# Kernel optimization log

Measured on AMD Instinct MI355X. Metric: run time of the kernel, lower is better.

## Reference

```python
import jax, jax.numpy as jnp
import numpy as np

B, D, CL, QL = 32, 128, 1024, 512


def setup_inputs() -> dict:
    key = jax.random.key(0)
    kC, kQ, kW = jax.random.split(key, 3)
    C = jax.random.normal(kC, (B, D, CL), dtype=jnp.float32)
    Q = jax.random.normal(kQ, (B, D, QL), dtype=jnp.float32)
    # xavier_normal_ on (B*CL, 1, 3D): std = sqrt(2 / (fan_in + fan_out)) = sqrt(2/(1+3D))
    std = (2.0 / (1.0 + 3.0 * D)) ** 0.5
    W = jax.random.normal(kW, (B * CL, 1, 3 * D), dtype=jnp.float32) * std
    return {"C": C, "Q": Q, "W": W}


def reference(C, Q, W):
    # C: (B, D, CL), Q: (B, D, QL), W: (B*CL, 1, 3D)
    b, d, cl = C.shape
    Ct = jnp.transpose(C, (0, 2, 1))   # (B, CL, D)
    Qt = jnp.transpose(Q, (0, 2, 1))   # (B, QL, D)
    Wr = W.reshape(b, cl, 3 * d)
    wq, wc, wqc = Wr[..., :d], Wr[..., d:2 * d], Wr[..., 2 * d:]
    # Trilinear similarity: S[b,c,q] = wq[b,c].Q[b,q] + wc[b,c].C[b,c] + wqc[b,c].(C[b,c]*Q[b,q])
    S = (jnp.einsum('bcd,bqd->bcq', wq, Qt)
         + jnp.sum(wc * Ct, axis=-1, keepdims=True)
         + jnp.einsum('bcd,bqd->bcq', wqc * Ct, Qt))   # (B, CL, QL)
    S1 = jax.nn.softmax(S, axis=2)  # over queries
    S2 = jax.nn.softmax(S, axis=1)  # over context
    A = jnp.einsum('bcq,bqd->bcd', S1, Qt)             # (B, CL, D)
    # B = (S1 @ S2^T) @ C, reassociated as S1 @ (S2^T @ C) to avoid (CL,CL) intermediate
    S2tC = jnp.einsum('bkq,bkd->bqd', S2, Ct)          # (B, QL, D)
    Bm = jnp.einsum('bcq,bqd->bcd', S1, S2tC)          # (B, CL, D)
    out = jnp.concatenate([Ct, A, Ct * A, Ct * Bm], axis=2)  # (B, CL, 4D)
    # dropout is identity in eval mode
    return jnp.transpose(out, (0, 2, 1))               # (B, 4D, CL)
```

## Files before the change

### kernel.cpp

```cpp
#include <hip/hip_runtime.h>
#include <hip/hip_bf16.h>
#include <cstddef>

#define B_  32
#define D_  128
#define CL_ 1024
#define QL_ 512

using short8  = __attribute__((ext_vector_type(8))) short;
using short4v = __attribute__((ext_vector_type(4))) short;
using float4v = __attribute__((ext_vector_type(4))) float;

__device__ __forceinline__ unsigned short f2bf(float f) {
    unsigned int u = __float_as_uint(f);
    u += 0x7FFFu + ((u >> 16) & 1u);
    return (unsigned short)(u >> 16);
}
__device__ __forceinline__ float bf2f(unsigned short h) {
    return __uint_as_float(((unsigned int)h) << 16);
}

__global__ __launch_bounds__(256) void k_u_bias(const float* __restrict__ C,
                                                const float* __restrict__ W,
                                                unsigned short* __restrict__ U,
                                                float* __restrict__ bias,
                                                unsigned short* __restrict__ Cbf) {
    int b  = blockIdx.y;
    int c0 = blockIdx.x * 32;
    int tid = threadIdx.x;

    __shared__ float tile[128][33];
    __shared__ float bred[32][9];

    for (int pass = 0; pass < 16; ++pass) {
        int d = pass * 8 + (tid >> 5);
        int c = tid & 31;
        float v = C[((size_t)(b * D_ + d)) * CL_ + c0 + c];
        tile[d][c] = v;
        Cbf[((size_t)(b * D_ + d)) * CL_ + c0 + c] = f2bf(v);
    }
    __syncthreads();

    int tc    = tid >> 3;
    int lane8 = tid & 7;
    int c     = c0 + tc;
    size_t wbase = ((size_t)(b * CL_ + c)) * (3 * D_);
    size_t ubase = ((size_t)(b * CL_ + c)) * D_;

    float bpart = 0.f;
    #pragma unroll
    for (int i = 0; i < 4; ++i) {
        int d = i * 32 + lane8 * 4;
        float4 wq4  = *(const float4*)(W + wbase + d);
        float4 wc4  = *(const float4*)(W + wbase + D_ + d);
        float4 wqc4 = *(const float4*)(W + wbase + 2 * D_ + d);
        float ct0 = tile[d + 0][tc], ct1 = tile[d + 1][tc];
        float ct2 = tile[d + 2][tc], ct3 = tile[d + 3][tc];
        short4v u;
        u[0] = (short)f2bf(wq4.x + wqc4.x * ct0);
        u[1] = (short)f2bf(wq4.y + wqc4.y * ct1);
        u[2] = (short)f2bf(wq4.z + wqc4.z * ct2);
        u[3] = (short)f2bf(wq4.w + wqc4.w * ct3);
        *(short4v*)(U + ubase + d) = u;
        bpart += wc4.x * ct0 + wc4.y * ct1 + wc4.z * ct2 + wc4.w * ct3;
    }
    bred[tc][lane8] = bpart;
    __syncthreads();
    if (lane8 == 0) {
        float s = 0.f;
        for (int i = 0; i < 8; ++i) s += bred[tc][i];
        bias[b * CL_ + c] = s;
    }
}

__global__ __launch_bounds__(256) void k_qt(const float* __restrict__ Q,
                                            unsigned short* __restrict__ Qt,
                                            unsigned short* __restrict__ Qbf) {
    int b  = blockIdx.z;
    int d0 = blockIdx.y * 64;
    int q0 = blockIdx.x * 64;
    int tid = threadIdx.x;
    __shared__ float t[64][65];
    for (int p = 0; p < 16; ++p) {
        int d = p * 4 + (tid >> 6);
        int q = tid & 63;
        float v = Q[((size_t)(b * D_ + d0 + d)) * QL_ + q0 + q];
        t[d][q] = v;
        Qbf[((size_t)(b * D_ + d0 + d)) * QL_ + q0 + q] = f2bf(v);
    }
    __syncthreads();
    for (int p = 0; p < 16; ++p) {
        int q  = p * 4 + (tid >> 6);
        int dd = tid & 63;
        Qt[((size_t)(b * QL_ + q0 + q)) * D_ + d0 + dd] = f2bf(t[dd][q]);
    }
}

__global__ __launch_bounds__(256) void k_gs2(const unsigned short* __restrict__ Ubf,
                                             const unsigned short* __restrict__ Qtbf,
                                             const float* __restrict__ bias,
                                             unsigned short* __restrict__ Sbf,
                                             float* __restrict__ rmax,
                                             float* __restrict__ rinv,
                                             float* __restrict__ pcmax,
                                             float* __restrict__ pcsum) {
    int mt = blockIdx.x;
    int b  = blockIdx.y;
    int m0 = mt * 64;
    int tid  = threadIdx.x;
    int lane = tid & 63, wave = tid >> 6;
    int wm = wave >> 1, wn = wave & 1;
    int quad = lane >> 4, l15 = lane & 15;

    __shared__ __align__(16) short As[64][136];
    __shared__ __align__(16) short Bs[64][136];
    __shared__ float sbias[64];
    __shared__ float rmw[2][64], rsw[2][64];
    __shared__ float cmw[2][64], csw[2][64];

    const unsigned short* Ab = Ubf  + ((size_t)(b * CL_ + m0)) * D_;
    const unsigned short* Bb = Qtbf + ((size_t)(b * QL_)) * D_;

    #pragma unroll
    for (int i = 0; i < 4; ++i) {
        int flat = tid + i * 256;
        int row = flat >> 4, col = (flat & 15) * 8;
        *(short8*)&As[row][col] = *(const short8*)(Ab + (size_t)row * D_ + col);
    }
    if (tid < 64) sbias[tid] = bias[b * CL_ + m0 + tid];

    float rm_run[2][4], rs_run[2][4];
    #pragma unroll
    for (int fi = 0; fi < 2; ++fi)
        #pragma unroll
        for (int rr = 0; rr < 4; ++rr) { rm_run[fi][rr] = -1e30f; rs_run[fi][rr] = 0.f; }

    for (int chunk = 0; chunk < 8; ++chunk) {
        __syncthreads();
        #pragma unroll
        for (int i = 0; i < 4; ++i) {
            int flat = tid + i * 256;
            int row = flat >> 4, col = (flat & 15) * 8;
            *(short8*)&Bs[row][col] = *(const short8*)(Bb + (size_t)(chunk * 64 + row) * D_ + col);
        }
        __syncthreads();

        float4v acc[2][2] = {};
        #pragma unroll
        for (int ks = 0; ks < 128; ks += 32) {
            short8 af0 = *(const short8*)&As[wm * 32 + l15][ks + quad * 8];
            short8 af1 = *(const short8*)&As[wm * 32 + 16 + l15][ks + quad * 8];
            short8 bf0 = *(const short8*)&Bs[wn * 32 + l15][ks + quad * 8];
            short8 bf1 = *(const short8*)&Bs[wn * 32 + 16 + l15][ks + quad * 8];
            acc[0][0] = __builtin_amdgcn_mfma_f32_16x16x32_bf16(af0, bf0, acc[0][0], 0, 0, 0);
            acc[0][1] = __builtin_amdgcn_mfma_f32_16x16x32_bf16(af0, bf1, acc[0][1], 0, 0, 0);
            acc[1][0] = __builtin_amdgcn_mfma_f32_16x16x32_bf16(af1, bf0, acc[1][0], 0, 0, 0);
            acc[1][1] = __builtin_amdgcn_mfma_f32_16x16x32_bf16(af1, bf1, acc[1][1], 0, 0, 0);
        }

        float v[2][2][4];
        #pragma unroll
        for (int fi = 0; fi < 2; ++fi)
            #pragma unroll
            for (int fj = 0; fj < 2; ++fj)
                #pragma unroll
                for (int rr = 0; rr < 4; ++rr) {
                    int mloc = wm * 32 + fi * 16 + quad * 4 + rr;
                    float x = acc[fi][fj][rr] + sbias[mloc];
                    v[fi][fj][rr] = x;
                    int nloc = wn * 32 + fj * 16 + l15;
                    Sbf[((size_t)(b * CL_ + m0 + mloc)) * QL_ + chunk * 64 + nloc] = f2bf(x);
                }

        #pragma unroll
        for (int fi = 0; fi < 2; ++fi)
            #pragma unroll
            for (int rr = 0; rr < 4; ++rr) {
                float v0 = v[fi][0][rr], v1 = v[fi][1][rr];
                float nm = fmaxf(rm_run[fi][rr], fmaxf(v0, v1));
                rs_run[fi][rr] = rs_run[fi][rr] * __expf(rm_run[fi][rr] - nm)
                               + __expf(v0 - nm) + __expf(v1 - nm);
                rm_run[fi][rr] = nm;
            }

        #pragma unroll
        for (int fj = 0; fj < 2; ++fj) {
            float cm = v[0][fj][0];
            #pragma unroll
            for (int fi = 0; fi < 2; ++fi)
                #pragma unroll
                for (int rr = 0; rr < 4; ++rr) cm = fmaxf(cm, v[fi][fj][rr]);
            float cs = 0.f;
            #pragma unroll
            for (int fi = 0; fi < 2; ++fi)
                #pragma unroll
                for (int rr = 0; rr < 4; ++rr) cs += __expf(v[fi][fj][rr] - cm);
            #pragma unroll
            for (int off = 16; off <= 32; off <<= 1) {
                float om = __shfl_xor(cm, off);
                float os = __shfl_xor(cs, off);
                float nm = fmaxf(cm, om);
                cs = cs * __expf(cm - nm) + os * __expf(om - nm);
                cm = nm;
            }
            if (quad == 0) {
                int col = wn * 32 + fj * 16 + l15;
                cmw[wm][col] = cm;
                csw[wm][col] = cs;
            }
        }
        __syncthreads();
        if (tid < 64) {
            float m0v = cmw[0][tid], s0v = csw[0][tid];
            float m1v = cmw[1][tid], s1v = csw[1][tid];
            float nm = fmaxf(m0v, m1v);
            float ss = s0v * __expf(m0v - nm) + s1v * __expf(m1v - nm);
            size_t pi = ((size_t)(b * 16 + mt)) * QL_ + chunk * 64 + tid;
            pcmax[pi] = nm;
            pcsum[pi] = ss;
        }
    }

    #pragma unroll
    for (int off = 1; off <= 8; off <<= 1)
        #pragma unroll
        for (int fi = 0; fi < 2; ++fi)
            #pragma unroll
            for (int rr = 0; rr < 4; ++rr) {
                float om = __shfl_xor(rm_run[fi][rr], off);
                float os = __shfl_xor(rs_run[fi][rr], off);
                float nm = fmaxf(rm_run[fi][rr], om);
                rs_run[fi][rr] = rs_run[fi][rr] * __expf(rm_run[fi][rr] - nm)
                               + os * __expf(om - nm);
                rm_run[fi][rr] = nm;
            }
    if (l15 == 0) {
        #pragma unroll
        for (int fi = 0; fi < 2; ++fi)
            #pragma unroll
            for (int rr = 0; rr < 4; ++rr) {
                int m = wm * 32 + fi * 16 + quad * 4 + rr;
                rmw[wn][m] = rm_run[fi][rr];
                rsw[wn][m] = rs_run[fi][rr];
            }
    }
    __syncthreads();
    if (tid < 64) {
        float m0v = rmw[0][tid], s0v = rsw[0][tid];
        float m1v = rmw[1][tid], s1v = rsw[1][tid];
        float nm = fmaxf(m0v, m1v);
        float ss = s0v * __expf(m0v - nm) + s1v * __expf(m1v - nm);
        rmax[b * CL_ + m0 + tid] = nm;
        rinv[b * CL_ + m0 + tid] = 1.0f / ss;
    }
}

__global__ __launch_bounds__(256) void k_gp(const unsigned short* __restrict__ Cbf,
                                            const unsigned short* __restrict__ Sbf,
                                            const float* __restrict__ pcmax,
                                            const float* __restrict__ pcsum,
                                            unsigned short* __restrict__ Pbf) {
    int b  = blockIdx.y;
    int q0 = blockIdx.x * 32;

    int tid  = threadIdx.x;
    int lane = tid & 63, wave = tid >> 6;
    int quad = lane >> 4, l15 = lane & 15;

    __shared__ __align__(16) short As[128][72];
    __shared__ __align__(16) short Bs[32][72];
    __shared__ float scm[32], sci[32];

    if (tid < 32) {
        float M = -1e30f, SS = 0.f;
        #pragma unroll
        for (int ch = 0; ch < 16; ++ch) {
            size_t idx = ((size_t)(b * 16 + ch)) * QL_ + q0 + tid;
            float m = pcmax[idx], s = pcsum[idx];
            float nM = fmaxf(M, m);
            SS = SS * __expf(M - nM) + s * __expf(m - nM);
            M = nM;
        }
        scm[tid] = M;
        sci[tid] = 1.0f / SS;
    }
    __syncthreads();

    const unsigned short* Cb = Cbf + (size_t)b * D_ * CL_;
    const unsigned short* Sb = Sbf + (size_t)b * CL_ * QL_;

    int arow = tid >> 3;
    int acol = (tid & 7) * 8;
    int srow = tid >> 4;
    int uq   = tid & 15;

    float4v acc[2][2] = {};

    for (int k0 = 0; k0 < CL_; k0 += 64) {
        #pragma unroll
        for (int p = 0; p < 4; ++p) {
            int row = p * 32 + arow;
            *(short8*)&As[row][acol] = *(const short8*)(Cb + (size_t)row * CL_ + k0 + acol);
        }
        #pragma unroll
        for (int p = 0; p < 4; ++p) {
            int crow = p * 16 + srow;
            unsigned int raw = *(const unsigned int*)(Sb + (size_t)(k0 + crow) * QL_ + q0 + 2 * uq);
            float v0 = __expf(bf2f((unsigned short)(raw & 0xFFFF)) - scm[2 * uq]) * sci[2 * uq];
            float v1 = __expf(bf2f((unsigned short)(raw >> 16)) - scm[2 * uq + 1]) * sci[2 * uq + 1];
            Bs[2 * uq][crow]     = (short)f2bf(v0);
            Bs[2 * uq + 1][crow] = (short)f2bf(v1);
        }
        __syncthreads();
        #pragma unroll
        for (int ks = 0; ks < 64; ks += 32) {
            short8 a0 = *(const short8*)&As[wave * 32 + l15][ks + quad * 8];
            short8 a1 = *(const short8*)&As[wave * 32 + 16 + l15][ks + quad * 8];
            short8 b0 = *(const short8*)&Bs[l15][ks + quad * 8];
            short8 b1 = *(const short8*)&Bs[16 + l15][ks + quad * 8];
            acc[0][0] = __builtin_amdgcn_mfma_f32_16x16x32_bf16(a0, b0, acc[0][0], 0, 0, 0);
            acc[0][1] = __builtin_amdgcn_mfma_f32_16x16x32_bf16(a0, b1, acc[0][1], 0, 0, 0);
            acc[1][0] = __builtin_amdgcn_mfma_f32_16x16x32_bf16(a1, b0, acc[1][0], 0, 0, 0);
            acc[1][1] = __builtin_amdgcn_mfma_f32_16x16x32_bf16(a1, b1, acc[1][1], 0, 0, 0);
        }
        __syncthreads();
    }

    #pragma unroll
    for (int fi = 0; fi < 2; ++fi)
        #pragma unroll
        for (int fj = 0; fj < 2; ++fj)
            #pragma unroll
            for (int rr = 0; rr < 4; ++rr) {
                int d = wave * 32 + fi * 16 + quad * 4 + rr;
                int q = q0 + fj * 16 + l15;
                Pbf[((size_t)(b * D_ + d)) * QL_ + q] = f2bf(acc[fi][fj][rr]);
            }
}

__global__ __launch_bounds__(256) void k_av2(const unsigned short* __restrict__ Qbf,
                                             const unsigned short* __restrict__ Pbf,
                                             const unsigned short* __restrict__ Sbf,
                                             const float* __restrict__ rmax,
                                             const float* __restrict__ rinv,
                                             const float* __restrict__ C,
                                             float* __restrict__ out) {
    int b  = blockIdx.y;
    int n0 = blockIdx.x * 64;

    int tid  = threadIdx.x;
    int lane = tid & 63, wave = tid >> 6;
    int wm = wave >> 1, wn = wave & 1;
    int quad = lane >> 4, l15 = lane & 15;

    __shared__ __align__(16) short AsQ[128][72];
    __shared__ __align__(16) short AsP[128][72];
    __shared__ __align__(16) short Bs[64][72];
    __shared__ float srm[64], sri[64];

    if (tid < 64) {
        srm[tid] = rmax[b * CL_ + n0 + tid];
        sri[tid] = rinv[b * CL_ + n0 + tid];
    }
    __syncthreads();

    const unsigned short* Qb = Qbf + (size_t)b * D_ * QL_;
    const unsigned short* Pb = Pbf + (size_t)b * D_ * QL_;
    const unsigned short* Sb = Sbf + ((size_t)(b * CL_ + n0)) * QL_;

    int arow = tid >> 3;
    int acol = (tid & 7) * 8;
    int brow = tid >> 2;
    int bcol = (tid & 3) * 16;
    float brm = srm[brow], bri = sri[brow];

    float4v accQ[4][2] = {};
    float4v accP[4][2] = {};

    for (int k0 = 0; k0 < QL_; k0 += 64) {
        #pragma unroll
        for (int p = 0; p < 4; ++p) {
            int row = p * 32 + arow;
            *(short8*)&AsQ[row][acol] = *(const short8*)(Qb + (size_t)row * QL_ + k0 + acol);
            *(short8*)&AsP[row][acol] = *(const short8*)(Pb + (size_t)row * QL_ + k0 + acol);
        }
        #pragma unroll
        for (int h = 0; h < 2; ++h) {
            uint4 raw = *(const uint4*)(Sb + (size_t)brow * QL_ + k0 + bcol + h * 8);
            unsigned int rw[4] = {raw.x, raw.y, raw.z, raw.w};
            short8 v;
            #pragma unroll
            for (int j = 0; j < 8; ++j) {
                unsigned short bits = (unsigned short)((rw[j >> 1] >> ((j & 1) * 16)) & 0xFFFF);
                v[j] = (short)f2bf(__expf(bf2f(bits) - brm) * bri);
            }
            *(short8*)&Bs[brow][bcol + h * 8] = v;
        }
        __syncthreads();
        #pragma unroll
        for (int ks = 0; ks < 64; ks += 32) {
            short8 b0 = *(const short8*)&Bs[wn * 32 + l15][ks + quad * 8];
            short8 b1 = *(const short8*)&Bs[wn * 32 + 16 + l15][ks + quad * 8];
            #pragma unroll
            for (int fi = 0; fi < 4; ++fi) {
                short8 aq = *(const short8*)&AsQ[wm * 64 + fi * 16 + l15][ks + quad * 8];
                accQ[fi][0] = __builtin_amdgcn_mfma_f32_16x16x32_bf16(aq, b0, accQ[fi][0], 0, 0, 0);
                accQ[fi][1] = __builtin_amdgcn_mfma_f32_16x16x32_bf16(aq, b1, accQ[fi][1], 0, 0, 0);
            }
            #pragma unroll
            for (int fi = 0; fi < 4; ++fi) {
                short8 ap = *(const short8*)&AsP[wm * 64 + fi * 16 + l15][ks + quad * 8];
                accP[fi][0] = __builtin_amdgcn_mfma_f32_16x16x32_bf16(ap, b0, accP[fi][0], 0, 0, 0);
                accP[fi][1] = __builtin_amdgcn_mfma_f32_16x16x32_bf16(ap, b1, accP[fi][1], 0, 0, 0);
            }
        }
        __syncthreads();
    }

    #pragma unroll
    for (int fi = 0; fi < 4; ++fi)
        #pragma unroll
        for (int fj = 0; fj < 2; ++fj)
            #pragma unroll
            for (int rr = 0; rr < 4; ++rr) {
                int d = wm * 64 + fi * 16 + quad * 4 + rr;
                int c = n0 + wn * 32 + fj * 16 + l15;
                float ct = C[((size_t)(b * D_ + d)) * CL_ + c];
                float vq = accQ[fi][fj][rr];
                float vp = accP[fi][fj][rr];
                size_t ob = ((size_t)(b * 4 * D_ + d)) * CL_ + c;
                out[ob]                        = ct;
                out[ob + (size_t)D_ * CL_]     = vq;
                out[ob + 2 * (size_t)D_ * CL_] = ct * vq;
                out[ob + 3 * (size_t)D_ * CL_] = ct * vp;
            }
}

extern "C" void kernel_launch(void* const* d_in, const int* in_sizes, int n_in,
                              void* d_out, int out_size, void* d_ws, size_t ws_size,
                              hipStream_t stream) {
    const float* C = (const float*)d_in[0];
    const float* Q = (const float*)d_in[1];
    const float* W = (const float*)d_in[2];
    float* out = (float*)d_out;

    unsigned short* Ubf  = (unsigned short*)d_ws;
    unsigned short* Qtbf = Ubf  + (size_t)B_ * CL_ * D_;
    unsigned short* Qbf  = Qtbf + (size_t)B_ * QL_ * D_;
    unsigned short* Cbf  = Qbf  + (size_t)B_ * D_ * QL_;
    unsigned short* Pbf  = Cbf  + (size_t)B_ * D_ * CL_;
    unsigned short* Sbf  = Pbf  + (size_t)B_ * D_ * QL_;
    float* bias  = (float*)(Sbf + (size_t)B_ * CL_ * QL_);
    float* rmax  = bias  + (size_t)B_ * CL_;
    float* rinv  = rmax  + (size_t)B_ * CL_;
    float* pcmax = rinv  + (size_t)B_ * CL_;
    float* pcsum = pcmax + (size_t)B_ * 16 * QL_;

    k_u_bias<<<dim3(CL_ / 32, B_), 256, 0, stream>>>(C, W, Ubf, bias, Cbf);
    k_qt<<<dim3(QL_ / 64, D_ / 64, B_), 256, 0, stream>>>(Q, Qtbf, Qbf);
    k_gs2<<<dim3(16, B_), 256, 0, stream>>>(Ubf, Qtbf, bias, Sbf, rmax, rinv, pcmax, pcsum);
    k_gp<<<dim3(QL_ / 32, B_), 256, 0, stream>>>(Cbf, Sbf, pcmax, pcsum, Pbf);
    k_av2<<<dim3(CL_ / 64, B_), 256, 0, stream>>>(Qbf, Pbf, Sbf, rmax, rinv, C, out);
}
```

Before: 200.3 us.

## Fuse score GEMM with column-softmax P=C·S2 via online softmax per query tile

```diff
diff --git a/kernel.cpp b/kernel.cpp
--- a/kernel.cpp
+++ b/kernel.cpp
@@ -96,257 +96,207 @@
     }
 }
 
-__global__ __launch_bounds__(256) void k_gs2(const unsigned short* __restrict__ Ubf,
+__global__ __launch_bounds__(256) void k_sgp(const unsigned short* __restrict__ Ubf,
                                              const unsigned short* __restrict__ Qtbf,
+                                             const unsigned short* __restrict__ Cbf,
                                              const float* __restrict__ bias,
                                              unsigned short* __restrict__ Sbf,
-                                             float* __restrict__ rmax,
-                                             float* __restrict__ rinv,
-                                             float* __restrict__ pcmax,
-                                             float* __restrict__ pcsum) {
-    int mt = blockIdx.x;
-    int b  = blockIdx.y;
-    int m0 = mt * 64;
+                                             unsigned short* __restrict__ Pbf,
+                                             float* __restrict__ prmax,
+                                             float* __restrict__ prsum) {
+    int i = blockIdx.x;
+    int slot = i >> 3;
+    int b  = (i & 7) + 8 * (slot >> 4);
+    int qt = slot & 15;
+    int q0 = qt * 32;
+
     int tid  = threadIdx.x;
     int lane = tid & 63, wave = tid >> 6;
     int wm = wave >> 1, wn = wave & 1;
     int quad = lane >> 4, l15 = lane & 15;
 
-    __shared__ __align__(16) short As[64][136];
-    __shared__ __align__(16) short Bs[64][136];
+    __shared__ __align__(16) short Qts[32][136];
+    __shared__ __align__(16) short Us[64][136];
+    __shared__ __align__(16) short Cs[128][72];
+    __shared__ __align__(16) short Ps[32][72];
     __shared__ float sbias[64];
+    __shared__ float scm[32], scs[32], sfac[32];
+    __shared__ float cmw[2][32], csw[2][32];
     __shared__ float rmw[2][64], rsw[2][64];
-    __shared__ float cmw[2][64], csw[2][64];
-
-    const unsigned short* Ab = Ubf  + ((size_t)(b * CL_ + m0)) * D_;
-    const unsigned short* Bb = Qtbf + ((size_t)(b * QL_)) * D_;
 
     #pragma unroll
-    for (int i = 0; i < 4; ++i) {
-        int flat = tid + i * 256;
+    for (int p = 0; p < 2; ++p) {
+        int flat = tid + p * 256;
         int row = flat >> 4, col = (flat & 15) * 8;
-        *(short8*)&As[row][col] = *(const short8*)(Ab + (size_t)row * D_ + col);
-    }
-    if (tid < 64) sbias[tid] = bias[b * CL_ + m0 + tid];
-
-    float rm_run[2][4], rs_run[2][4];
-    #pragma unroll
-    for (int fi = 0; fi < 2; ++fi)
-        #pragma unroll
-        for (int rr = 0; rr < 4; ++rr) { rm_run[fi][rr] = -1e30f; rs_run[fi][rr] = 0.f; }
-
-    for (int chunk = 0; chunk < 8; ++chunk) {
-        __syncthreads();
-        #pragma unroll
-        for (int i = 0; i < 4; ++i) {
-            int flat = tid + i * 256;
+        *(short8*)&Qts[row][col] = *(const short8*)(Qtbf + ((size_t)(b * QL_ + q0 + row)) * D_ + col);
+    }
+    if (tid < 32) { scm[tid] = -1e30f; scs[tid] = 0.f; }
+
+    const unsigned short* Ub = Ubf + (size_t)b * CL_ * D_;
+    const unsigned short* Cb = Cbf + (size_t)b * D_ * CL_;
+
+    int q_loc = wn * 16 + l15;
+    float4v acc_p[4] = {};
+
+    for (int ch = 0; ch < 16; ++ch) {
+        int c0 = ch * 64;
+        __syncthreads();
+        #pragma unroll
+        for (int p = 0; p < 4; ++p) {
+            int flat = tid + p * 256;
             int row = flat >> 4, col = (flat & 15) * 8;
-            *(short8*)&Bs[row][col] = *(const short8*)(Bb + (size_t)(chunk * 64 + row) * D_ + col);
-        }
-        __syncthreads();
-
-        float4v acc[2][2] = {};
+            *(short8*)&Us[row][col] = *(const short8*)(Ub + (size_t)(c0 + row) * D_ + col);
+        }
+        #pragma unroll
+        for (int p = 0; p < 4; ++p) {
+            int flat = tid + p * 256;
+            int row = flat >> 3, col = (flat & 7) * 8;
+            *(short8*)&Cs[row][col] = *(const short8*)(Cb + (size_t)row * CL_ + c0 + col);
+        }
+        if (tid < 64) sbias[tid] = bias[b * CL_ + c0 + tid];
+        __syncthreads();
+
+        float4v acc_s[2] = {};
         #pragma unroll
         for (int ks = 0; ks < 128; ks += 32) {
-            short8 af0 = *(const short8*)&As[wm * 32 + l15][ks + quad * 8];
-            short8 af1 = *(const short8*)&As[wm * 32 + 16 + l15][ks + quad * 8];
-            short8 bf0 = *(const short8*)&Bs[wn * 32 + l15][ks + quad * 8];
-            short8 bf1 = *(const short8*)&Bs[wn * 32 + 16 + l15][ks + quad * 8];
-            acc[0][0] = __builtin_amdgcn_mfma_f32_16x16x32_bf16(af0, bf0, acc[0][0], 0, 0, 0);
-            acc[0][1] = __builtin_amdgcn_mfma_f32_16x16x32_bf16(af0, bf1, acc[0][1], 0, 0, 0);
-            acc[1][0] = __builtin_amdgcn_mfma_f32_16x16x32_bf16(af1, bf0, acc[1][0], 0, 0, 0);
-            acc[1][1] = __builtin_amdgcn_mfma_f32_16x16x32_bf16(af1, bf1, acc[1][1], 0, 0, 0);
-        }
-
-        float v[2][2][4];
-        #pragma unroll
-        for (int fi = 0; fi < 2; ++fi)
-            #pragma unroll
-            for (int fj = 0; fj < 2; ++fj)
+            short8 bq = *(const short8*)&Qts[q_loc][ks + quad * 8];
+            short8 a0 = *(const short8*)&Us[wm * 32 + l15][ks + quad * 8];
+            short8 a1 = *(const short8*)&Us[wm * 32 + 16 + l15][ks + quad * 8];
+            acc_s[0] = __builtin_amdgcn_mfma_f32_16x16x32_bf16(a0, bq, acc_s[0], 0, 0, 0);
+            acc_s[1] = __builtin_amdgcn_mfma_f32_16x16x32_bf16(a1, bq, acc_s[1], 0, 0, 0);
+        }
+
+        float v[2][4];
+        #pragma unroll
+        for (int fi = 0; fi < 2; ++fi)
+            #pragma unroll
+            for (int rr = 0; rr < 4; ++rr) {
+                int c_loc = wm * 32 + fi * 16 + quad * 4 + rr;
+                float x = acc_s[fi][rr] + sbias[c_loc];
+                v[fi][rr] = x;
+                Sbf[((size_t)(b * CL_ + c0 + c_loc)) * QL_ + q0 + q_loc] = f2bf(x);
+            }
+
+        float rm[2][4], rs[2][4];
+        #pragma unroll
+        for (int fi = 0; fi < 2; ++fi)
+            #pragma unroll
+            for (int rr = 0; rr < 4; ++rr) rm[fi][rr] = v[fi][rr];
+        #pragma unroll
+        for (int off = 1; off <= 8; off <<= 1)
+            #pragma unroll
+            for (int fi = 0; fi < 2; ++fi)
+                #pragma unroll
+                for (int rr = 0; rr < 4; ++rr)
+                    rm[fi][rr] = fmaxf(rm[fi][rr], __shfl_xor(rm[fi][rr], off));
+        #pragma unroll
+        for (int fi = 0; fi < 2; ++fi)
+            #pragma unroll
+            for (int rr = 0; rr < 4; ++rr) rs[fi][rr] = __expf(v[fi][rr] - rm[fi][rr]);
+        #pragma unroll
+        for (int off = 1; off <= 8; off <<= 1)
+            #pragma unroll
+            for (int fi = 0; fi < 2; ++fi)
+                #pragma unroll
+                for (int rr = 0; rr < 4; ++rr)
+                    rs[fi][rr] += __shfl_xor(rs[fi][rr], off);
+        if (l15 == 0) {
+            #pragma unroll
+            for (int fi = 0; fi < 2; ++fi)
                 #pragma unroll
                 for (int rr = 0; rr < 4; ++rr) {
-                    int mloc = wm * 32 + fi * 16 + quad * 4 + rr;
-                    float x = acc[fi][fj][rr] + sbias[mloc];
-                    v[fi][fj][rr] = x;
-                    int nloc = wn * 32 + fj * 16 + l15;
-                    Sbf[((size_t)(b * CL_ + m0 + mloc)) * QL_ + chunk * 64 + nloc] = f2bf(x);
+                    int c_loc = wm * 32 + fi * 16 + quad * 4 + rr;
+                    rmw[wn][c_loc] = rm[fi][rr];
+                    rsw[wn][c_loc] = rs[fi][rr];
                 }
-
+        }
+
+        float cm = v[0][0];
+        #pragma unroll
+        for (int fi = 0; fi < 2; ++fi)
+            #pragma unroll
+            for (int rr = 0; rr < 4; ++rr) cm = fmaxf(cm, v[fi][rr]);
+        float cs = 0.f;
+        #pragma unroll
+        for (int fi = 0; fi < 2; ++fi)
+            #pragma unroll
+            for (int rr = 0; rr < 4; ++rr) cs += __expf(v[fi][rr] - cm);
+        #pragma unroll
+        for (int off = 16; off <= 32; off <<= 1) {
+            float om = __shfl_xor(cm, off);
+            float os = __shfl_xor(cs, off);
+            float nm = fmaxf(cm, om);
+            cs = cs * __expf(cm - nm) + os * __expf(om - nm);
+            cm = nm;
+        }
+        if (quad == 0) { cmw[wm][q_loc] = cm; csw[wm][q_loc] = cs; }
+        __syncthreads();
+
+        if (tid < 64) {
+            float m0 = rmw[0][tid], m1 = rmw[1][tid];
+            float nm = fmaxf(m0, m1);
+            float ss = rsw[0][tid] * __expf(m0 - nm) + rsw[1][tid] * __expf(m1 - nm);
+            prmax[((size_t)(b * 16 + qt)) * CL_ + c0 + tid] = nm;
+            prsum[((size_t)(b * 16 + qt)) * CL_ + c0 + tid] = ss;
+        }
+        if (tid < 32) {
+            float m0 = cmw[0][tid], m1 = cmw[1][tid];
+            float mm = fmaxf(m0, m1);
+            float ss = csw[0][tid] * __expf(m0 - mm) + csw[1][tid] * __expf(m1 - mm);
+            float om = scm[tid];
+            float nm = fmaxf(om, mm);
+            float f  = __expf(om - nm);
+            sfac[tid] = f;
+            scs[tid] = scs[tid] * f + ss * __expf(mm - nm);
+            scm[tid] = nm;
+        }
+        __syncthreads();
+
+        float f = sfac[q_loc];
+        float cmn = scm[q_loc];
+        #pragma unroll
+        for (int fi = 0; fi < 4; ++fi) acc_p[fi] *= f;
         #pragma unroll
         for (int fi = 0; fi < 2; ++fi)
             #pragma unroll
             for (int rr = 0; rr < 4; ++rr) {
-                float v0 = v[fi][0][rr], v1 = v[fi][1][rr];
-                float nm = fmaxf(rm_run[fi][rr], fmaxf(v0, v1));
-                rs_run[fi][rr] = rs_run[fi][rr] * __expf(rm_run[fi][rr] - nm)
-                               + __expf(v0 - nm) + __expf(v1 - nm);
-                rm_run[fi][rr] = nm;
-            }
-
-        #pragma unroll
-        for (int fj = 0; fj < 2; ++fj) {
-            float cm = v[0][fj][0];
-            #pragma unroll
-            for (int fi = 0; fi < 2; ++fi)
-                #pragma unroll
-                for (int rr = 0; rr < 4; ++rr) cm = fmaxf(cm, v[fi][fj][rr]);
-            float cs = 0.f;
-            #pragma unroll
-            for (int fi = 0; fi < 2; ++fi)
-                #pragma unroll
-                for (int rr = 0; rr < 4; ++rr) cs += __expf(v[fi][fj][rr] - cm);
-            #pragma unroll
-            for (int off = 16; off <= 32; off <<= 1) {
-                float om = __shfl_xor(cm, off);
-                float os = __shfl_xor(cs, off);
-                float nm = fmaxf(cm, om);
-                cs = cs * __expf(cm - nm) + os * __expf(om - nm);
-                cm = nm;
-            }
-            if (quad == 0) {
-                int col = wn * 32 + fj * 16 + l15;
-                cmw[wm][col] = cm;
-                csw[wm][col] = cs;
-            }
-        }
-        __syncthreads();
-        if (tid < 64) {
-            float m0v = cmw[0][tid], s0v = csw[0][tid];
-            float m1v = cmw[1][tid], s1v = csw[1][tid];
-            float nm = fmaxf(m0v, m1v);
-            float ss = s0v * __expf(m0v - nm) + s1v * __expf(m1v - nm);
-            size_t pi = ((size_t)(b * 16 + mt)) * QL_ + chunk * 64 + tid;
-            pcmax[pi] = nm;
-            pcsum[pi] = ss;
-        }
-    }
-
+                int c_loc = wm * 32 + fi * 16 + quad * 4 + rr;
+                Ps[q_loc][c_loc] = (short)f2bf(__expf(v[fi][rr] - cmn));
+            }
+        __syncthreads();
+
+        #pragma unroll
+        for (int ks = 0; ks < 64; ks += 32) {
+            short8 bp = *(const short8*)&Ps[q_loc][ks + quad * 8];
+            #pragma unroll
+            for (int fi = 0; fi < 4; ++fi) {
+                short8 a = *(const short8*)&Cs[wm * 64 + fi * 16 + l15][ks + quad * 8];
+                acc_p[fi] = __builtin_amdgcn_mfma_f32_16x16x32_bf16(a, bp, acc_p[fi], 0, 0, 0);
+            }
+        }
+    }
+
+    float sci = 1.0f / scs[q_loc];
     #pragma unroll
-    for (int off = 1; off <= 8; off <<= 1)
-        #pragma unroll
-        for (int fi = 0; fi < 2; ++fi)
-            #pragma unroll
-            for (int rr = 0; rr < 4; ++rr) {
-                float om = __shfl_xor(rm_run[fi][rr], off);
-                float os = __shfl_xor(rs_run[fi][rr], off);
-                float nm = fmaxf(rm_run[fi][rr], om);
-                rs_run[fi][rr] = rs_run[fi][rr] * __expf(rm_run[fi][rr] - nm)
-                               + os * __expf(om - nm);
-                rm_run[fi][rr] = nm;
-            }
-    if (l15 == 0) {
-        #pragma unroll
-        for (int fi = 0; fi < 2; ++fi)
-            #pragma unroll
-            for (int rr = 0; rr < 4; ++rr) {
-                int m = wm * 32 + fi * 16 + quad * 4 + rr;
-                rmw[wn][m] = rm_run[fi][rr];
-                rsw[wn][m] = rs_run[fi][rr];
-            }
-    }
-    __syncthreads();
-    if (tid < 64) {
-        float m0v = rmw[0][tid], s0v = rsw[0][tid];
-        float m1v = rmw[1][tid], s1v = rsw[1][tid];
-        float nm = fmaxf(m0v, m1v);
-        float ss = s0v * __expf(m0v - nm) + s1v * __expf(m1v - nm);
-        rmax[b * CL_ + m0 + tid] = nm;
-        rinv[b * CL_ + m0 + tid] = 1.0f / ss;
-    }
-}
-
-__global__ __launch_bounds__(256) void k_gp(const unsigned short* __restrict__ Cbf,
-                                            const unsigned short* __restrict__ Sbf,
-                                            const float* __restrict__ pcmax,
-                                            const float* __restrict__ pcsum,
-                                            unsigned short* __restrict__ Pbf) {
-    int b  = blockIdx.y;
-    int q0 = blockIdx.x * 32;
-
-    int tid  = threadIdx.x;
-    int lane = tid & 63, wave = tid >> 6;
-    int quad = lane >> 4, l15 = lane & 15;
-
-    __shared__ __align__(16) short As[128][72];
-    __shared__ __align__(16) short Bs[32][72];
-    __shared__ float scm[32], sci[32];
-
-    if (tid < 32) {
-        float M = -1e30f, SS = 0.f;
-        #pragma unroll
-        for (int ch = 0; ch < 16; ++ch) {
-            size_t idx = ((size_t)(b * 16 + ch)) * QL_ + q0 + tid;
-            float m = pcmax[idx], s = pcsum[idx];
-            float nM = fmaxf(M, m);
-            SS = SS * __expf(M - nM) + s * __expf(m - nM);
-            M = nM;
-        }
-        scm[tid] = M;
-        sci[tid] = 1.0f / SS;
-    }
-    __syncthreads();
-
-    const unsigned short* Cb = Cbf + (size_t)b * D_ * CL_;
-    const unsigned short* Sb = Sbf + (size_t)b * CL_ * QL_;
-
-    int arow = tid >> 3;
-    int acol = (tid & 7) * 8;
-    int srow = tid >> 4;
-    int uq   = tid & 15;
-
-    float4v acc[2][2] = {};
-
-    for (int k0 = 0; k0 < CL_; k0 += 64) {
-        #pragma unroll
-        for (int p = 0; p < 4; ++p) {
-            int row = p * 32 + arow;
-            *(short8*)&As[row][acol] = *(const short8*)(Cb + (size_t)row * CL_ + k0 + acol);
-        }
-        #pragma unroll
-        for (int p = 0; p < 4; ++p) {
-            int crow = p * 16 + srow;
-            unsigned int raw = *(const unsigned int*)(Sb + (size_t)(k0 + crow) * QL_ + q0 + 2 * uq);
-            float v0 = __expf(bf2f((unsigned short)(raw & 0xFFFF)) - scm[2 * uq]) * sci[2 * uq];
-            float v1 = __expf(bf2f((unsigned short)(raw >> 16)) - scm[2 * uq + 1]) * sci[2 * uq + 1];
-            Bs[2 * uq][crow]     = (short)f2bf(v0);
-            Bs[2 * uq + 1][crow] = (short)f2bf(v1);
-        }
-        __syncthreads();
-        #pragma unroll
-        for (int ks = 0; ks < 64; ks += 32) {
-            short8 a0 = *(const short8*)&As[wave * 32 + l15][ks + quad * 8];
-            short8 a1 = *(const short8*)&As[wave * 32 + 16 + l15][ks + quad * 8];
-            short8 b0 = *(const short8*)&Bs[l15][ks + quad * 8];
-            short8 b1 = *(const short8*)&Bs[16 + l15][ks + quad * 8];
-            acc[0][0] = __builtin_amdgcn_mfma_f32_16x16x32_bf16(a0, b0, acc[0][0], 0, 0, 0);
-            acc[0][1] = __builtin_amdgcn_mfma_f32_16x16x32_bf16(a0, b1, acc[0][1], 0, 0, 0);
-            acc[1][0] = __builtin_amdgcn_mfma_f32_16x16x32_bf16(a1, b0, acc[1][0], 0, 0, 0);
-            acc[1][1] = __builtin_amdgcn_mfma_f32_16x16x32_bf16(a1, b1, acc[1][1], 0, 0, 0);
-        }
-        __syncthreads();
-    }
-
-    #pragma unroll
-    for (int fi = 0; fi < 2; ++fi)
-        #pragma unroll
-        for (int fj = 0; fj < 2; ++fj)
-            #pragma unroll
-            for (int rr = 0; rr < 4; ++rr) {
-                int d = wave * 32 + fi * 16 + quad * 4 + rr;
-                int q = q0 + fj * 16 + l15;
-                Pbf[((size_t)(b * D_ + d)) * QL_ + q] = f2bf(acc[fi][fj][rr]);
-            }
+    for (int fi = 0; fi < 4; ++fi)
+        #pragma unroll
+        for (int rr = 0; rr < 4; ++rr) {
+            int d = wm * 64 + fi * 16 + quad * 4 + rr;
+            Pbf[((size_t)(b * D_ + d)) * QL_ + q0 + q_loc] = f2bf(acc_p[fi][rr] * sci);
+        }
 }
 
 __global__ __launch_bounds__(256) void k_av2(const unsigned short* __restrict__ Qbf,
                                              const unsigned short* __restrict__ Pbf,
                                              const unsigned short* __restrict__ Sbf,
-                                             const float* __restrict__ rmax,
-                                             const float* __restrict__ rinv,
+                                             const float* __restrict__ prmax,
+                                             const float* __restrict__ prsum,
                                              const float* __restrict__ C,
                                              float* __restrict__ out) {
-    int b  = blockIdx.y;
-    int n0 = blockIdx.x * 64;
+    int i = blockIdx.x;
+    int slot = i >> 3;
+    int b  = (i & 7) + 8 * (slot >> 4);
+    int n0 = (slot & 15) * 64;
 
     int tid  = threadIdx.x;
     int lane = tid & 63, wave = tid >> 6;
@@ -359,8 +309,17 @@
     __shared__ float srm[64], sri[64];
 
     if (tid < 64) {
-        srm[tid] = rmax[b * CL_ + n0 + tid];
-        sri[tid] = rinv[b * CL_ + n0 + tid];
+        float M = -1e30f, S = 0.f;
+        #pragma unroll
+        for (int qt = 0; qt < 16; ++qt) {
+            float m = prmax[((size_t)(b * 16 + qt)) * CL_ + n0 + tid];
+            float s = prsum[((size_t)(b * 16 + qt)) * CL_ + n0 + tid];
+            float nM = fmaxf(M, m);
+            S = S * __expf(M - nM) + s * __expf(m - nM);
+            M = nM;
+        }
+        srm[tid] = M;
+        sri[tid] = 1.0f / S;
     }
     __syncthreads();
 
@@ -388,13 +347,13 @@
         for (int h = 0; h < 2; ++h) {
             uint4 raw = *(const uint4*)(Sb + (size_t)brow * QL_ + k0 + bcol + h * 8);
             unsigned int rw[4] = {raw.x, raw.y, raw.z, raw.w};
-            short8 v;
+            short8 vv;
             #pragma unroll
             for (int j = 0; j < 8; ++j) {
                 unsigned short bits = (unsigned short)((rw[j >> 1] >> ((j & 1) * 16)) & 0xFFFF);
-                v[j] = (short)f2bf(__expf(bf2f(bits) - brm) * bri);
-            }
-            *(short8*)&Bs[brow][bcol + h * 8] = v;
+                vv[j] = (short)f2bf(__expf(bf2f(bits) - brm) * bri);
+            }
+            *(short8*)&Bs[brow][bcol + h * 8] = vv;
         }
         __syncthreads();
         #pragma unroll
@@ -451,14 +410,11 @@
     unsigned short* Pbf  = Cbf  + (size_t)B_ * D_ * CL_;
     unsigned short* Sbf  = Pbf  + (size_t)B_ * D_ * QL_;
     float* bias  = (float*)(Sbf + (size_t)B_ * CL_ * QL_);
-    float* rmax  = bias  + (size_t)B_ * CL_;
-    float* rinv  = rmax  + (size_t)B_ * CL_;
-    float* pcmax = rinv  + (size_t)B_ * CL_;
-    float* pcsum = pcmax + (size_t)B_ * 16 * QL_;
+    float* prmax = bias  + (size_t)B_ * CL_;
+    float* prsum = prmax + (size_t)B_ * 16 * CL_;
 
     k_u_bias<<<dim3(CL_ / 32, B_), 256, 0, stream>>>(C, W, Ubf, bias, Cbf);
     k_qt<<<dim3(QL_ / 64, D_ / 64, B_), 256, 0, stream>>>(Q, Qtbf, Qbf);
-    k_gs2<<<dim3(16, B_), 256, 0, stream>>>(Ubf, Qtbf, bias, Sbf, rmax, rinv, pcmax, pcsum);
-    k_gp<<<dim3(QL_ / 32, B_), 256, 0, stream>>>(Cbf, Sbf, pcmax, pcsum, Pbf);
-    k_av2<<<dim3(CL_ / 64, B_), 256, 0, stream>>>(Qbf, Pbf, Sbf, rmax, rinv, C, out);
-}
+    k_sgp<<<512, 256, 0, stream>>>(Ubf, Qtbf, Cbf, bias, Sbf, Pbf, prmax, prsum);
+    k_av2<<<512, 256, 0, stream>>>(Qbf, Pbf, Sbf, prmax, prsum, C, out);
+}
```

Result: slower. 218.0 us (+8.8%).
